# Optimization experiments

Measured on AMD Instinct MI355X. Metric: run time of the kernel, lower is better.

Reference implementation:

```python
import jax, jax.numpy as jnp
import numpy as np

B, H, W = 4, 64, 64
INPLANES, PLANES, G, K = 608, 152, 19, 3
KK = K * K
EPS = 1e-5


def conv2d(x, w, stride=1, padding=0, dilation=1):
    return jax.lax.conv_general_dilated(
        x, w, (stride, stride), [(padding, padding)] * 2,
        rhs_dilation=(dilation, dilation),
        dimension_numbers=("NCHW", "OIHW", "NCHW"))


def bn(x, g, b, m, v):
    # inference-mode batchnorm (affine with running stats)
    inv = g / jnp.sqrt(v + EPS)
    return x * inv[None, :, None, None] + (b - m * inv)[None, :, None, None]


def deform_conv(x, offset, w, pad=1, dil=1):
    # x: [B,C,H,W], offset: [B, 2*G*KK, H, W] ((dy,dx) pairs per group per tap), w: [Cout,C,K,K]
    Bs, C, Hh, Ww = x.shape
    Cg = C // G
    off = offset.reshape(Bs, G, KK, 2, Hh, Ww)
    ky, kx = jnp.meshgrid(jnp.arange(K), jnp.arange(K), indexing="ij")
    base_y = (jnp.arange(Hh) - pad)[None, None, None, :, None] + (dil * ky.reshape(-1))[None, None, :, None, None]
    base_x = (jnp.arange(Ww) - pad)[None, None, None, None, :] + (dil * kx.reshape(-1))[None, None, :, None, None]
    ys = base_y + off[:, :, :, 0]  # [B,G,KK,H,W]
    xs = base_x + off[:, :, :, 1]
    y0 = jnp.floor(ys)
    x0 = jnp.floor(xs)
    wy = ys - y0
    wx = xs - x0
    y0i = y0.astype(jnp.int32)
    x0i = x0.astype(jnp.int32)
    xf = x.reshape(Bs, G, Cg, Hh * Ww)

    def gather(yi, xi, wgt):
        valid = ((yi >= 0) & (yi < Hh) & (xi >= 0) & (xi < Ww)).astype(x.dtype)
        idx = jnp.clip(yi, 0, Hh - 1) * Ww + jnp.clip(xi, 0, Ww - 1)
        idxf = jnp.broadcast_to(idx.reshape(Bs, G, 1, KK * Hh * Ww), (Bs, G, Cg, KK * Hh * Ww))
        g = jnp.take_along_axis(xf, idxf, axis=3).reshape(Bs, G, Cg, KK, Hh, Ww)
        return g * (wgt * valid)[:, :, None]

    samp = (gather(y0i, x0i, (1 - wy) * (1 - wx))
            + gather(y0i, x0i + 1, (1 - wy) * wx)
            + gather(y0i + 1, x0i, wy * (1 - wx))
            + gather(y0i + 1, x0i + 1, wy * wx))  # [B,G,Cg,KK,H,W]
    wr = w.reshape(w.shape[0], G, Cg, KK)
    return jnp.einsum("bgckhw,ogck->bohw", samp, wr)


def setup_inputs() -> dict:
    key = jax.random.key(0)
    ks = jax.random.split(key, 8)
    d = {}
    d["x"] = jax.random.normal(ks[0], (B, INPLANES, H, W), jnp.float32)
    d["conv1_w"] = jax.random.normal(ks[1], (PLANES, INPLANES, 1, 1), jnp.float32) * 0.05
    d["conv2_w"] = jax.random.normal(ks[2], (2 * G * KK, PLANES, 3, 3), jnp.float32) * 0.01
    d["dconv_w"] = jax.random.normal(ks[3], (PLANES, PLANES, 3, 3), jnp.float32) * 0.05
    d["conv3_w"] = jax.random.normal(ks[4], (4 * PLANES, PLANES, 1, 1), jnp.float32) * 0.05
    for i, (name, c) in enumerate([("bn1", PLANES), ("bn2", PLANES), ("bn3", 4 * PLANES)]):
        k1, k2, k3, k4 = jax.random.split(ks[5 + i], 4)
        d[name + "_g"] = jax.random.uniform(k1, (c,), jnp.float32, 0.5, 1.5)
        d[name + "_b"] = jax.random.normal(k2, (c,), jnp.float32) * 0.1
        d[name + "_m"] = jax.random.normal(k3, (c,), jnp.float32) * 0.1
        d[name + "_v"] = jax.random.uniform(k4, (c,), jnp.float32, 0.5, 1.5)
    return d


def reference(x, conv1_w, conv2_w, dconv_w, conv3_w,
              bn1_g, bn1_b, bn1_m, bn1_v,
              bn2_g, bn2_b, bn2_m, bn2_v,
              bn3_g, bn3_b, bn3_m, bn3_v):
    out = jax.nn.relu(conv2d(x, conv1_w))           # conv1 -> relu (order as in source)
    out = bn(out, bn1_g, bn1_b, bn1_m, bn1_v)       # -> bn1
    offset = conv2d(out, conv2_w, padding=1)         # offset-generating 3x3 conv
    out = deform_conv(out, offset, dconv_w)          # deformable 3x3 conv
    out = bn(jax.nn.relu(out), bn2_g, bn2_b, bn2_m, bn2_v)
    out = bn(conv2d(out, conv3_w), bn3_g, bn3_b, bn3_m, bn3_v)
    return jax.nn.relu(out + x)
```

## Files before the change

### kernel.cpp

```cpp
#include <hip/hip_runtime.h>

#define EPSV 1e-5f

typedef __bf16 bf16_t;
typedef __bf16 bf16x8 __attribute__((ext_vector_type(8)));
typedef float f32x4 __attribute__((ext_vector_type(4)));

__device__ inline bf16x8 bzero8() {
  bf16x8 z;
#pragma unroll
  for (int i = 0; i < 8; i++) z[i] = (bf16_t)0.f;
  return z;
}

__device__ inline f32x4 mfma16(bf16x8 a, bf16x8 b, f32x4 c) {
  return __builtin_amdgcn_mfma_f32_16x16x32_bf16(a, b, c, 0, 0, 0);
}

#define W1E (160 * 608)
#define W2E (384 * 1376)
#define WDE (192 * 1376)
#define W3E (640 * 160)

__global__ __launch_bounds__(256) void prep_weights(
    const float* __restrict__ w1, const float* __restrict__ w2,
    const float* __restrict__ wd, const float* __restrict__ w3,
    bf16_t* __restrict__ w1b, bf16_t* __restrict__ w2b,
    bf16_t* __restrict__ wdb, bf16_t* __restrict__ w3b) {
  int i = blockIdx.x * 256 + threadIdx.x;
  float v = 0.f;
  if (i < W1E) {
    int oc = i / 608, ic = i % 608;
    if (oc < 152) v = w1[oc * 608 + ic];
    w1b[i] = (bf16_t)v;
  } else if (i < W1E + W2E) {
    int j = i - W1E;
    int oc = j / 1376, k = j % 1376;
    if (oc < 342 && k < 1368) {
      int t = k / 152, ic = k % 152;
      v = w2[(oc * 152 + ic) * 9 + t];
    }
    w2b[j] = (bf16_t)v;
  } else if (i < W1E + W2E + WDE) {
    int j = i - W1E - W2E;
    int o = j / 1376, k = j % 1376;
    if (o < 152 && k < 1368) {
      int t = k / 152, ic = k % 152;
      v = wd[(o * 152 + ic) * 9 + t];
    }
    wdb[j] = (bf16_t)v;
  } else if (i < W1E + W2E + WDE + W3E) {
    int j = i - W1E - W2E - WDE;
    int oc = j / 160, ic = j % 160;
    if (oc < 608 && ic < 152) v = w3[oc * 152 + ic];
    w3b[j] = (bf16_t)v;
  }
}

__global__ void prep_bn(const float* g1, const float* b1, const float* m1, const float* v1,
                        const float* g2, const float* b2, const float* m2, const float* v2,
                        const float* g3, const float* b3, const float* m3, const float* v3,
                        float* __restrict__ bnc) {
  int i = threadIdx.x;
  if (i < 152) {
    float inv = g1[i] / sqrtf(v1[i] + EPSV);
    bnc[i] = inv;
    bnc[152 + i] = b1[i] - m1[i] * inv;
    float inv2 = g2[i] / sqrtf(v2[i] + EPSV);
    bnc[304 + i] = inv2;
    bnc[456 + i] = b2[i] - m2[i] * inv2;
  }
  if (i < 608) {
    float inv3 = g3[i] / sqrtf(v3[i] + EPSV);
    bnc[608 + i] = inv3;
    bnc[1216 + i] = b3[i] - m3[i] * inv3;
  }
}

__global__ __launch_bounds__(256) void s1_conv1(const float* __restrict__ x,
                                                const bf16_t* __restrict__ w1b,
                                                const float* __restrict__ bnc,
                                                bf16_t* __restrict__ out1) {
  __shared__ bf16_t t1[32 * 616];
  int tid = threadIdx.x;
  int px0 = blockIdx.x * 32;
  int b = px0 >> 12, sp0 = px0 & 4095;
  for (int task = tid; task < 608 * 8; task += 256) {
    int c = task >> 3, i4 = task & 7;
    f32x4 v = *(const f32x4*)(x + (((size_t)(b * 608 + c)) << 12) + sp0 + i4 * 4);
#pragma unroll
    for (int i = 0; i < 4; i++) t1[(i4 * 4 + i) * 616 + c] = (bf16_t)v[i];
  }
  __syncthreads();
  int wid = tid >> 6, lane = tid & 63, q = lane >> 4, lr = lane & 15;
  int mw = wid & 1, nw = wid >> 1;
  f32x4 acc[5];
#pragma unroll
  for (int n = 0; n < 5; n++) acc[n] = (f32x4){0.f, 0.f, 0.f, 0.f};
  for (int kk = 0; kk < 19; kk++) {
    int k0 = kk * 32 + q * 8;
    bf16x8 a = *(const bf16x8*)(t1 + (mw * 16 + lr) * 616 + k0);
#pragma unroll
    for (int n = 0; n < 5; n++) {
      bf16x8 bf = *(const bf16x8*)(w1b + (nw * 80 + n * 16 + lr) * 608 + k0);
      acc[n] = mfma16(a, bf, acc[n]);
    }
  }
#pragma unroll
  for (int n = 0; n < 5; n++) {
    int oc = nw * 80 + n * 16 + lr;
    if (oc < 152) {
      float inv = bnc[oc], beta = bnc[152 + oc];
#pragma unroll
      for (int i = 0; i < 4; i++) {
        int p = px0 + mw * 16 + q * 4 + i;
        float v = fmaxf(acc[n][i], 0.f) * inv + beta;
        out1[(size_t)p * 152 + oc] = (bf16_t)v;
      }
    }
  }
}

__global__ __launch_bounds__(256, 4) void s2_offs(const bf16_t* __restrict__ out1,
                                                  const bf16_t* __restrict__ w2b,
                                                  float* __restrict__ offs) {
  __shared__ bf16_t t2[3 * 34 * 156];
  int tid = threadIdx.x;
  int nh = blockIdx.x & 1;
  int rest = blockIdx.x >> 1;
  int xh = rest & 1, y = (rest >> 1) & 63, b = rest >> 7;
  const bf16_t* ob = out1 + (((size_t)b) << 12) * 152;
  int x0 = xh * 32 - 1;
  for (int task = tid; task < 3 * 34 * 19; task += 256) {
    int j = task / 646, r = task % 646;
    int xi = r / 19, cb = r % 19;
    int yy = y + j - 1, xx = x0 + xi;
    bf16x8 v = bzero8();
    if (yy >= 0 && yy < 64 && xx >= 0 && xx < 64)
      v = *(const bf16x8*)(ob + (size_t)(yy * 64 + xx) * 152 + cb * 8);
    *(bf16x8*)(t2 + (j * 34 + xi) * 156 + cb * 8) = v;
  }
  __syncthreads();
  int wid = tid >> 6, lane = tid & 63, q = lane >> 4, lr = lane & 15;
  int ncol0 = nh * 192 + wid * 48;
  f32x4 acc[2][3];
#pragma unroll
  for (int m = 0; m < 2; m++)
#pragma unroll
    for (int n = 0; n < 3; n++) acc[m][n] = (f32x4){0.f, 0.f, 0.f, 0.f};
  const bf16_t* wb = w2b + (size_t)(ncol0 + lr) * 1376;
#pragma unroll
  for (int kk = 0; kk < 43; kk++) {
    int k0 = kk * 32 + q * 8;
    bf16x8 bfr[3];
#pragma unroll
    for (int n = 0; n < 3; n++)
      bfr[n] = *(const bf16x8*)(wb + (size_t)(n * 16) * 1376 + k0);
    bf16x8 a[2];
    if (k0 < 1368) {
      int t = k0 / 152, c0 = k0 - t * 152;
      int dy = t / 3, dxp1 = t - dy * 3;
#pragma unroll
      for (int m = 0; m < 2; m++)
        a[m] = *(const bf16x8*)(t2 + (dy * 34 + m * 16 + lr + dxp1) * 156 + c0);
    } else {
      a[0] = bzero8();
      a[1] = bzero8();
    }
#pragma unroll
    for (int n = 0; n < 3; n++)
#pragma unroll
      for (int m = 0; m < 2; m++) acc[m][n] = mfma16(a[m], bfr[n], acc[m][n]);
  }
#pragma unroll
  for (int n = 0; n < 3; n++) {
    int col = ncol0 + n * 16 + lr;
    if (col < 342) {
#pragma unroll
      for (int m = 0; m < 2; m++)
#pragma unroll
        for (int i = 0; i < 4; i++) {
          int p = (b << 12) + y * 64 + xh * 32 + m * 16 + q * 4 + i;
          offs[(size_t)p * 344 + col] = acc[m][n][i];
        }
    }
  }
}

__global__ __launch_bounds__(256, 8) void s3a_sample(const bf16_t* __restrict__ out1,
                                                     const float* __restrict__ offs,
                                                     bf16_t* __restrict__ samp,
                                                     int p_base) {
  int task = blockIdx.x * 256 + threadIdx.x;
  int lp = task / 171, s = task - lp * 171;
  int t = s / 19, g = s - t * 19;
  int p = p_base + lp;
  int b = p >> 12, y = (p >> 6) & 63, xc = p & 63;
  int ky = t / 3, kx = t - ky * 3;
  float2 ov = *(const float2*)(offs + (size_t)p * 344 + g * 18 + t * 2);
  float ys = (float)(y - 1 + ky) + ov.x;
  float xs = (float)(xc - 1 + kx) + ov.y;
  float y0f = floorf(ys), x0f = floorf(xs);
  float wy = ys - y0f, wx = xs - x0f;
  int y0 = (int)y0f, x0 = (int)x0f;
  int y1 = y0 + 1, x1 = x0 + 1;
  int y0c = min(max(y0, 0), 63), x0c = min(max(x0, 0), 63);
  int y1c = min(max(y1, 0), 63), x1c = min(max(x1, 0), 63);
  float vy0 = (y0 == y0c) ? 1.f : 0.f;
  float vy1 = (y1 == y1c) ? 1.f : 0.f;
  float vx0 = (x0 == x0c) ? 1.f : 0.f;
  float vx1 = (x1 == x1c) ? 1.f : 0.f;
  float w00 = (1.f - wy) * (1.f - wx) * vy0 * vx0;
  float w01 = (1.f - wy) * wx * vy0 * vx1;
  float w10 = wy * (1.f - wx) * vy1 * vx0;
  float w11 = wy * wx * vy1 * vx1;
  const bf16_t* bg = out1 + (((size_t)b << 12) * 152) + g * 8;
  bf16x8 c00 = *(const bf16x8*)(bg + (size_t)(y0c * 64 + x0c) * 152);
  bf16x8 c01 = *(const bf16x8*)(bg + (size_t)(y0c * 64 + x1c) * 152);
  bf16x8 c10 = *(const bf16x8*)(bg + (size_t)(y1c * 64 + x0c) * 152);
  bf16x8 c11 = *(const bf16x8*)(bg + (size_t)(y1c * 64 + x1c) * 152);
  bf16x8 o;
#pragma unroll
  for (int i = 0; i < 8; i++) {
    float f = w00 * (float)c00[i];
    f = fmaf(w01, (float)c01[i], f);
    f = fmaf(w10, (float)c10[i], f);
    f = fmaf(w11, (float)c11[i], f);
    o[i] = (bf16_t)f;
  }
  *(bf16x8*)(samp + (size_t)lp * 1376 + t * 152 + g * 8) = o;
  if (s == 170) *(bf16x8*)(samp + (size_t)lp * 1376 + 1368) = bzero8();
}

__global__ __launch_bounds__(512, 4) void s3b_gemm(const bf16_t* __restrict__ samp,
                                                   const bf16_t* __restrict__ wdb,
                                                   const float* __restrict__ bnc,
                                                   bf16_t* __restrict__ a2,
                                                   int p_base) {
  int tid = threadIdx.x;
  int wid = tid >> 6, lane = tid & 63, q = lane >> 4, lr = lane & 15;
  int mw = wid & 1, nw = wid >> 1;
  int lrow = blockIdx.x * 32 + mw * 16;
  const bf16_t* arow = samp + (size_t)(lrow + lr) * 1376;
  const bf16_t* wb = wdb + (size_t)(nw * 48 + lr) * 1376;
  f32x4 acc[3];
#pragma unroll
  for (int n = 0; n < 3; n++) acc[n] = (f32x4){0.f, 0.f, 0.f, 0.f};
#pragma unroll
  for (int kk = 0; kk < 43; kk++) {
    int k0 = kk * 32 + q * 8;
    bf16x8 a = *(const bf16x8*)(arow + k0);
#pragma unroll
    for (int n = 0; n < 3; n++) {
      bf16x8 bf = *(const bf16x8*)(wb + (size_t)(n * 16) * 1376 + k0);
      acc[n] = mfma16(a, bf, acc[n]);
    }
  }
#pragma unroll
  for (int n = 0; n < 3; n++) {
    int oc = nw * 48 + n * 16 + lr;
    if (oc < 152) {
      float inv = bnc[304 + oc], beta = bnc[456 + oc];
#pragma unroll
      for (int i = 0; i < 4; i++) {
        int p = p_base + lrow + q * 4 + i;
        float v = fmaxf(acc[n][i], 0.f) * inv + beta;
        a2[(size_t)p * 152 + oc] = (bf16_t)v;
      }
    }
  }
}

__global__ __launch_bounds__(256) void s4_conv3(const bf16_t* __restrict__ a2,
                                                const bf16_t* __restrict__ w3b,
                                                const float* __restrict__ bnc,
                                                const float* __restrict__ x,
                                                float* __restrict__ out) {
  int tid = threadIdx.x;
  int wid = tid >> 6, lane = tid & 63, q = lane >> 4, lr = lane & 15;
  int p0 = blockIdx.x * 16;
  int b = p0 >> 12, sp0 = p0 & 4095;
  f32x4 acc[10];
#pragma unroll
  for (int n = 0; n < 10; n++) acc[n] = (f32x4){0.f, 0.f, 0.f, 0.f};
  for (int kk = 0; kk < 5; kk++) {
    int k0 = kk * 32 + q * 8;
    bf16x8 a = (k0 < 152) ? *(const bf16x8*)(a2 + (size_t)(p0 + lr) * 152 + k0) : bzero8();
#pragma unroll
    for (int n = 0; n < 10; n++) {
      bf16x8 bf = *(const bf16x8*)(w3b + (size_t)(wid * 160 + n * 16 + lr) * 160 + k0);
      acc[n] = mfma16(a, bf, acc[n]);
    }
  }
#pragma unroll
  for (int n = 0; n < 10; n++) {
    int oc = wid * 160 + n * 16 + lr;
    if (oc < 608) {
      float inv = bnc[608 + oc], beta = bnc[1216 + oc];
      size_t gi = (((size_t)(b * 608 + oc)) << 12) + sp0 + q * 4;
      f32x4 xr = *(const f32x4*)(x + gi);
      f32x4 o;
#pragma unroll
      for (int i = 0; i < 4; i++) o[i] = fmaxf(acc[n][i] * inv + beta + xr[i], 0.f);
      *(f32x4*)(out + gi) = o;
    }
  }
}

extern "C" void kernel_launch(void* const* d_in, const int* in_sizes, int n_in,
                              void* d_out, int out_size, void* d_ws, size_t ws_size,
                              hipStream_t stream) {
  const float* x = (const float*)d_in[0];
  const float* w1 = (const float*)d_in[1];
  const float* w2 = (const float*)d_in[2];
  const float* wd = (const float*)d_in[3];
  const float* w3 = (const float*)d_in[4];
  const float* g1 = (const float*)d_in[5];
  const float* b1 = (const float*)d_in[6];
  const float* m1 = (const float*)d_in[7];
  const float* v1 = (const float*)d_in[8];
  const float* g2 = (const float*)d_in[9];
  const float* b2 = (const float*)d_in[10];
  const float* m2 = (const float*)d_in[11];
  const float* v2 = (const float*)d_in[12];
  const float* g3 = (const float*)d_in[13];
  const float* b3 = (const float*)d_in[14];
  const float* m3 = (const float*)d_in[15];
  const float* v3 = (const float*)d_in[16];

  char* ws = (char*)d_ws;
  bf16_t* w1b = (bf16_t*)(ws + 0);
  bf16_t* w2b = (bf16_t*)(ws + 194560);
  bf16_t* wdb = (bf16_t*)(ws + 1251328);
  bf16_t* w3b = (bf16_t*)(ws + 1779712);
  float* bnc = (float*)(ws + 1984512);
  bf16_t* out1 = (bf16_t*)(ws + 1991808);
  float* offs = (float*)(ws + 6972544);
  bf16_t* a2 = (bf16_t*)(ws + 29516928);
  bf16_t* samp = (bf16_t*)(ws + 34497664);
  float* out = (float*)d_out;

  prep_weights<<<3876, 256, 0, stream>>>(w1, w2, wd, w3, w1b, w2b, wdb, w3b);
  prep_bn<<<1, 640, 0, stream>>>(g1, b1, m1, v1, g2, b2, m2, v2, g3, b3, m3, v3, bnc);
  s1_conv1<<<512, 256, 0, stream>>>(x, w1b, bnc, out1);
  s2_offs<<<1024, 256, 0, stream>>>(out1, w2b, offs);

  size_t base = 34497664;
  int nchunk = 1;
  if (ws_size < base + (size_t)16384 * 1376 * 2) nchunk = 4;
  if (nchunk == 4 && ws_size < base + (size_t)4096 * 1376 * 2) nchunk = 16;
  int npix = 16384 / nchunk;
  for (int c = 0; c < nchunk; c++) {
    s3a_sample<<<npix * 171 / 256, 256, 0, stream>>>(out1, offs, samp, c * npix);
    s3b_gemm<<<npix / 32, 512, 0, stream>>>(samp, wdb, bnc, a2, c * npix);
  }

  s4_conv3<<<1024, 256, 0, stream>>>(a2, w3b, bnc, x, out);
}
```

Measured before the change: 182.4 us.

## Fuse deformable sampling with GEMM via LDS and split-K partials reduced in conv3

Bilinear sampling and the deformable-conv GEMM now run in one kernel. Each block samples 16 pixels times 3 taps into shared memory and runs the MFMA on them, so the large bf16 sample buffer is never written to or read back from global memory. The K dimension is split three ways across blocks, which writes fp32 partial sums. conv3 then sums the partials and applies relu and bn2 on the fly. In exchange it adds fp32 partial traffic (3x16384x192 floats), a per-element bn lookup in conv3, and weight re-reads from global memory per small tile.

```diff
diff --git a/kernel.cpp b/kernel.cpp
--- a/kernel.cpp
+++ b/kernel.cpp
@@ -5,6 +5,7 @@
 typedef __bf16 bf16_t;
 typedef __bf16 bf16x8 __attribute__((ext_vector_type(8)));
 typedef float f32x4 __attribute__((ext_vector_type(4)));
+typedef float f32x8 __attribute__((ext_vector_type(8)));
 
 __device__ inline bf16x8 bzero8() {
   bf16x8 z;
@@ -19,7 +20,7 @@
 
 #define W1E (160 * 608)
 #define W2E (384 * 1376)
-#define WDE (192 * 1376)
+#define WDE (192 * 1440)
 #define W3E (640 * 160)
 
 __global__ __launch_bounds__(256) void prep_weights(
@@ -43,11 +44,9 @@
     w2b[j] = (bf16_t)v;
   } else if (i < W1E + W2E + WDE) {
     int j = i - W1E - W2E;
-    int o = j / 1376, k = j % 1376;
-    if (o < 152 && k < 1368) {
-      int t = k / 152, ic = k % 152;
-      v = wd[(o * 152 + ic) * 9 + t];
-    }
+    int o = j / 1440, k = j % 1440;
+    int t = k / 160, ic = k % 160;
+    if (o < 152 && ic < 152) v = wd[(o * 152 + ic) * 9 + t];
     wdb[j] = (bf16_t)v;
   } else if (i < W1E + W2E + WDE + W3E) {
     int j = i - W1E - W2E - WDE;
@@ -187,105 +186,123 @@
   }
 }
 
-__global__ __launch_bounds__(256, 8) void s3a_sample(const bf16_t* __restrict__ out1,
-                                                     const float* __restrict__ offs,
-                                                     bf16_t* __restrict__ samp,
-                                                     int p_base) {
-  int task = blockIdx.x * 256 + threadIdx.x;
-  int lp = task / 171, s = task - lp * 171;
-  int t = s / 19, g = s - t * 19;
-  int p = p_base + lp;
-  int b = p >> 12, y = (p >> 6) & 63, xc = p & 63;
-  int ky = t / 3, kx = t - ky * 3;
-  float2 ov = *(const float2*)(offs + (size_t)p * 344 + g * 18 + t * 2);
-  float ys = (float)(y - 1 + ky) + ov.x;
-  float xs = (float)(xc - 1 + kx) + ov.y;
-  float y0f = floorf(ys), x0f = floorf(xs);
-  float wy = ys - y0f, wx = xs - x0f;
-  int y0 = (int)y0f, x0 = (int)x0f;
-  int y1 = y0 + 1, x1 = x0 + 1;
-  int y0c = min(max(y0, 0), 63), x0c = min(max(x0, 0), 63);
-  int y1c = min(max(y1, 0), 63), x1c = min(max(x1, 0), 63);
-  float vy0 = (y0 == y0c) ? 1.f : 0.f;
-  float vy1 = (y1 == y1c) ? 1.f : 0.f;
-  float vx0 = (x0 == x0c) ? 1.f : 0.f;
-  float vx1 = (x1 == x1c) ? 1.f : 0.f;
-  float w00 = (1.f - wy) * (1.f - wx) * vy0 * vx0;
-  float w01 = (1.f - wy) * wx * vy0 * vx1;
-  float w10 = wy * (1.f - wx) * vy1 * vx0;
-  float w11 = wy * wx * vy1 * vx1;
-  const bf16_t* bg = out1 + (((size_t)b << 12) * 152) + g * 8;
-  bf16x8 c00 = *(const bf16x8*)(bg + (size_t)(y0c * 64 + x0c) * 152);
-  bf16x8 c01 = *(const bf16x8*)(bg + (size_t)(y0c * 64 + x1c) * 152);
-  bf16x8 c10 = *(const bf16x8*)(bg + (size_t)(y1c * 64 + x0c) * 152);
-  bf16x8 c11 = *(const bf16x8*)(bg + (size_t)(y1c * 64 + x1c) * 152);
-  bf16x8 o;
-#pragma unroll
-  for (int i = 0; i < 8; i++) {
-    float f = w00 * (float)c00[i];
-    f = fmaf(w01, (float)c01[i], f);
-    f = fmaf(w10, (float)c10[i], f);
-    f = fmaf(w11, (float)c11[i], f);
-    o[i] = (bf16_t)f;
-  }
-  *(bf16x8*)(samp + (size_t)lp * 1376 + t * 152 + g * 8) = o;
-  if (s == 170) *(bf16x8*)(samp + (size_t)lp * 1376 + 1368) = bzero8();
-}
-
-__global__ __launch_bounds__(512, 4) void s3b_gemm(const bf16_t* __restrict__ samp,
+__global__ __launch_bounds__(256, 8) void s3_dconv(const bf16_t* __restrict__ out1,
+                                                   const float* __restrict__ offs,
                                                    const bf16_t* __restrict__ wdb,
-                                                   const float* __restrict__ bnc,
-                                                   bf16_t* __restrict__ a2,
-                                                   int p_base) {
+                                                   float* __restrict__ p3) {
+  __shared__ bf16_t abuf[16 * 488];
   int tid = threadIdx.x;
+  int bi = blockIdx.x;
+  int kc = bi % 3, pt = bi / 3;
+  int row0 = pt * 16;
+  int bb = row0 >> 12;
+  const bf16_t* obase = out1 + (((size_t)bb << 12) * 152);
+  if (tid < 64) {
+    int t = tid >> 4, r = tid & 15;
+    int off = (t < 3) ? t * 160 + 152 : 480;
+    *(bf16x8*)(abuf + r * 488 + off) = bzero8();
+  }
+  int t0 = kc * 3;
+  for (int task = tid; task < 912; task += 256) {
+    int tl = task / 304;
+    int rem = task - tl * 304;
+    int r = rem / 19, g = rem - r * 19;
+    int t = t0 + tl;
+    int ky = t / 3, kx = t - ky * 3;
+    int p = row0 + r;
+    int y = (p >> 6) & 63, xc = p & 63;
+    float2 ov = *(const float2*)(offs + (size_t)p * 344 + g * 18 + t * 2);
+    float ys = (float)(y - 1 + ky) + ov.x;
+    float xs = (float)(xc - 1 + kx) + ov.y;
+    float y0f = floorf(ys), x0f = floorf(xs);
+    float wy = ys - y0f, wx = xs - x0f;
+    int y0 = (int)y0f, x0 = (int)x0f;
+    int y1 = y0 + 1, x1 = x0 + 1;
+    int y0c = min(max(y0, 0), 63), x0c = min(max(x0, 0), 63);
+    int y1c = min(max(y1, 0), 63), x1c = min(max(x1, 0), 63);
+    float vy0 = (y0 == y0c) ? 1.f : 0.f;
+    float vy1 = (y1 == y1c) ? 1.f : 0.f;
+    float vx0 = (x0 == x0c) ? 1.f : 0.f;
+    float vx1 = (x1 == x1c) ? 1.f : 0.f;
+    float w00 = (1.f - wy) * (1.f - wx) * vy0 * vx0;
+    float w01 = (1.f - wy) * wx * vy0 * vx1;
+    float w10 = wy * (1.f - wx) * vy1 * vx0;
+    float w11 = wy * wx * vy1 * vx1;
+    const bf16_t* bg = obase + g * 8;
+    bf16x8 c00 = *(const bf16x8*)(bg + (size_t)(y0c * 64 + x0c) * 152);
+    bf16x8 c01 = *(const bf16x8*)(bg + (size_t)(y0c * 64 + x1c) * 152);
+    bf16x8 c10 = *(const bf16x8*)(bg + (size_t)(y1c * 64 + x0c) * 152);
+    bf16x8 c11 = *(const bf16x8*)(bg + (size_t)(y1c * 64 + x1c) * 152);
+    bf16x8 o;
+#pragma unroll
+    for (int i = 0; i < 8; i++) {
+      float f = w00 * (float)c00[i];
+      f = fmaf(w01, (float)c01[i], f);
+      f = fmaf(w10, (float)c10[i], f);
+      f = fmaf(w11, (float)c11[i], f);
+      o[i] = (bf16_t)f;
+    }
+    *(bf16x8*)(abuf + r * 488 + tl * 160 + g * 8) = o;
+  }
+  __syncthreads();
   int wid = tid >> 6, lane = tid & 63, q = lane >> 4, lr = lane & 15;
-  int mw = wid & 1, nw = wid >> 1;
-  int lrow = blockIdx.x * 32 + mw * 16;
-  const bf16_t* arow = samp + (size_t)(lrow + lr) * 1376;
-  const bf16_t* wb = wdb + (size_t)(nw * 48 + lr) * 1376;
   f32x4 acc[3];
 #pragma unroll
   for (int n = 0; n < 3; n++) acc[n] = (f32x4){0.f, 0.f, 0.f, 0.f};
-#pragma unroll
-  for (int kk = 0; kk < 43; kk++) {
+  const bf16_t* wb = wdb + (size_t)(wid * 48 + lr) * 1440 + kc * 480;
+#pragma unroll
+  for (int kk = 0; kk < 15; kk++) {
     int k0 = kk * 32 + q * 8;
-    bf16x8 a = *(const bf16x8*)(arow + k0);
+    bf16x8 a = *(const bf16x8*)(abuf + lr * 488 + k0);
 #pragma unroll
     for (int n = 0; n < 3; n++) {
-      bf16x8 bf = *(const bf16x8*)(wb + (size_t)(n * 16) * 1376 + k0);
+      bf16x8 bf = *(const bf16x8*)(wb + (size_t)(n * 16) * 1440 + k0);
       acc[n] = mfma16(a, bf, acc[n]);
     }
   }
+  float* pp = p3 + ((size_t)kc * 16384 + row0) * 192;
 #pragma unroll
   for (int n = 0; n < 3; n++) {
-    int oc = nw * 48 + n * 16 + lr;
-    if (oc < 152) {
-      float inv = bnc[304 + oc], beta = bnc[456 + oc];
-#pragma unroll
-      for (int i = 0; i < 4; i++) {
-        int p = p_base + lrow + q * 4 + i;
-        float v = fmaxf(acc[n][i], 0.f) * inv + beta;
-        a2[(size_t)p * 152 + oc] = (bf16_t)v;
-      }
-    }
-  }
-}
-
-__global__ __launch_bounds__(256) void s4_conv3(const bf16_t* __restrict__ a2,
+    int col = wid * 48 + n * 16 + lr;
+#pragma unroll
+    for (int i = 0; i < 4; i++) {
+      int rr = q * 4 + i;
+      pp[(size_t)rr * 192 + col] = acc[n][i];
+    }
+  }
+}
+
+__global__ __launch_bounds__(256) void s4_conv3(const float* __restrict__ p3,
                                                 const bf16_t* __restrict__ w3b,
                                                 const float* __restrict__ bnc,
                                                 const float* __restrict__ x,
                                                 float* __restrict__ out) {
+  const size_t PSZ = (size_t)16384 * 192;
   int tid = threadIdx.x;
   int wid = tid >> 6, lane = tid & 63, q = lane >> 4, lr = lane & 15;
   int p0 = blockIdx.x * 16;
   int b = p0 >> 12, sp0 = p0 & 4095;
+  const float* pbase = p3 + (size_t)(p0 + lr) * 192;
   f32x4 acc[10];
 #pragma unroll
   for (int n = 0; n < 10; n++) acc[n] = (f32x4){0.f, 0.f, 0.f, 0.f};
+#pragma unroll
   for (int kk = 0; kk < 5; kk++) {
     int k0 = kk * 32 + q * 8;
-    bf16x8 a = (k0 < 152) ? *(const bf16x8*)(a2 + (size_t)(p0 + lr) * 152 + k0) : bzero8();
+    bf16x8 a;
+    if (k0 < 152) {
+      f32x8 s0 = *(const f32x8*)(pbase + k0);
+      f32x8 s1 = *(const f32x8*)(pbase + PSZ + k0);
+      f32x8 s2 = *(const f32x8*)(pbase + 2 * PSZ + k0);
+#pragma unroll
+      for (int i = 0; i < 8; i++) {
+        float s = s0[i] + s1[i] + s2[i];
+        float v = fmaxf(s, 0.f) * bnc[304 + k0 + i] + bnc[456 + k0 + i];
+        a[i] = (bf16_t)v;
+      }
+    } else {
+      a = bzero8();
+    }
 #pragma unroll
     for (int n = 0; n < 10; n++) {
       bf16x8 bf = *(const bf16x8*)(w3b + (size_t)(wid * 160 + n * 16 + lr) * 160 + k0);
@@ -332,28 +349,17 @@
   bf16_t* w1b = (bf16_t*)(ws + 0);
   bf16_t* w2b = (bf16_t*)(ws + 194560);
   bf16_t* wdb = (bf16_t*)(ws + 1251328);
-  bf16_t* w3b = (bf16_t*)(ws + 1779712);
-  float* bnc = (float*)(ws + 1984512);
-  bf16_t* out1 = (bf16_t*)(ws + 1991808);
-  float* offs = (float*)(ws + 6972544);
-  bf16_t* a2 = (bf16_t*)(ws + 29516928);
-  bf16_t* samp = (bf16_t*)(ws + 34497664);
+  bf16_t* w3b = (bf16_t*)(ws + 1804288);
+  float* bnc = (float*)(ws + 2009088);
+  bf16_t* out1 = (bf16_t*)(ws + 2016384);
+  float* offs = (float*)(ws + 6997120);
+  float* p3 = (float*)(ws + 29541504);
   float* out = (float*)d_out;
 
-  prep_weights<<<3876, 256, 0, stream>>>(w1, w2, wd, w3, w1b, w2b, wdb, w3b);
+  prep_weights<<<3924, 256, 0, stream>>>(w1, w2, wd, w3, w1b, w2b, wdb, w3b);
   prep_bn<<<1, 640, 0, stream>>>(g1, b1, m1, v1, g2, b2, m2, v2, g3, b3, m3, v3, bnc);
   s1_conv1<<<512, 256, 0, stream>>>(x, w1b, bnc, out1);
   s2_offs<<<1024, 256, 0, stream>>>(out1, w2b, offs);
-
-  size_t base = 34497664;
-  int nchunk = 1;
-  if (ws_size < base + (size_t)16384 * 1376 * 2) nchunk = 4;
-  if (nchunk == 4 && ws_size < base + (size_t)4096 * 1376 * 2) nchunk = 16;
-  int npix = 16384 / nchunk;
-  for (int c = 0; c < nchunk; c++) {
-    s3a_sample<<<npix * 171 / 256, 256, 0, stream>>>(out1, offs, samp, c * npix);
-    s3b_gemm<<<npix / 32, 512, 0, stream>>>(samp, wdb, bnc, a2, c * npix);
-  }
-
-  s4_conv3<<<1024, 256, 0, stream>>>(a2, w3b, bnc, x, out);
-}
+  s3_dconv<<<3072, 256, 0, stream>>>(out1, offs, wdb, p3);
+  s4_conv3<<<1024, 256, 0, stream>>>(p3, w3b, bnc, x, out);
+}
```

Result: slower. 194.7 us (+6.8%).

## Stage deform-conv GEMM A tiles in LDS with double buffering per tap

Applied to the files above, without the earlier changes.

The sampled-activation matrix is re-laid out so each of the 9 taps has its own 160-wide padded segment. The deformable-conv GEMM now stages each tap's 32-row A tile into double-buffered shared memory, so one block of 4 waves shares it. Each wave computes 32 rows by 48 columns, which doubles reuse of the weight fragments it loads from global memory. The chunked sample/GEMM loop and its workspace-size check are gone: the code now assumes the workspace can hold the full 16384x1440 buffer, and a2 reuses the out1 region. The trade-off is fewer waves per block, extra barriers, and a larger buffer written and read.

```diff
diff --git a/kernel.cpp b/kernel.cpp
--- a/kernel.cpp
+++ b/kernel.cpp
@@ -19,7 +19,7 @@
 
 #define W1E (160 * 608)
 #define W2E (384 * 1376)
-#define WDE (192 * 1376)
+#define WDE (192 * 1440)
 #define W3E (640 * 160)
 
 __global__ __launch_bounds__(256) void prep_weights(
@@ -43,11 +43,9 @@
     w2b[j] = (bf16_t)v;
   } else if (i < W1E + W2E + WDE) {
     int j = i - W1E - W2E;
-    int o = j / 1376, k = j % 1376;
-    if (o < 152 && k < 1368) {
-      int t = k / 152, ic = k % 152;
-      v = wd[(o * 152 + ic) * 9 + t];
-    }
+    int o = j / 1440, k = j % 1440;
+    int t = k / 160, ic = k % 160;
+    if (o < 152 && ic < 152) v = wd[(o * 152 + ic) * 9 + t];
     wdb[j] = (bf16_t)v;
   } else if (i < W1E + W2E + WDE + W3E) {
     int j = i - W1E - W2E - WDE;
@@ -189,15 +187,13 @@
 
 __global__ __launch_bounds__(256, 8) void s3a_sample(const bf16_t* __restrict__ out1,
                                                      const float* __restrict__ offs,
-                                                     bf16_t* __restrict__ samp,
-                                                     int p_base) {
+                                                     bf16_t* __restrict__ samp) {
   int task = blockIdx.x * 256 + threadIdx.x;
   int lp = task / 171, s = task - lp * 171;
   int t = s / 19, g = s - t * 19;
-  int p = p_base + lp;
-  int b = p >> 12, y = (p >> 6) & 63, xc = p & 63;
+  int b = lp >> 12, y = (lp >> 6) & 63, xc = lp & 63;
   int ky = t / 3, kx = t - ky * 3;
-  float2 ov = *(const float2*)(offs + (size_t)p * 344 + g * 18 + t * 2);
+  float2 ov = *(const float2*)(offs + (size_t)lp * 344 + g * 18 + t * 2);
   float ys = (float)(y - 1 + ky) + ov.x;
   float xs = (float)(xc - 1 + kx) + ov.y;
   float y0f = floorf(ys), x0f = floorf(xs);
@@ -228,45 +224,77 @@
     f = fmaf(w11, (float)c11[i], f);
     o[i] = (bf16_t)f;
   }
-  *(bf16x8*)(samp + (size_t)lp * 1376 + t * 152 + g * 8) = o;
-  if (s == 170) *(bf16x8*)(samp + (size_t)lp * 1376 + 1368) = bzero8();
-}
-
-__global__ __launch_bounds__(512, 4) void s3b_gemm(const bf16_t* __restrict__ samp,
+  *(bf16x8*)(samp + (size_t)lp * 1440 + t * 160 + g * 8) = o;
+  if (g == 18) *(bf16x8*)(samp + (size_t)lp * 1440 + t * 160 + 152) = bzero8();
+}
+
+__global__ __launch_bounds__(256, 4) void s3b_gemm(const bf16_t* __restrict__ samp,
                                                    const bf16_t* __restrict__ wdb,
                                                    const float* __restrict__ bnc,
-                                                   bf16_t* __restrict__ a2,
-                                                   int p_base) {
+                                                   bf16_t* __restrict__ a2) {
+  __shared__ bf16_t at[2][32 * 168];
   int tid = threadIdx.x;
+  int row0 = blockIdx.x * 32;
   int wid = tid >> 6, lane = tid & 63, q = lane >> 4, lr = lane & 15;
-  int mw = wid & 1, nw = wid >> 1;
-  int lrow = blockIdx.x * 32 + mw * 16;
-  const bf16_t* arow = samp + (size_t)(lrow + lr) * 1376;
-  const bf16_t* wb = wdb + (size_t)(nw * 48 + lr) * 1376;
-  f32x4 acc[3];
-#pragma unroll
-  for (int n = 0; n < 3; n++) acc[n] = (f32x4){0.f, 0.f, 0.f, 0.f};
-#pragma unroll
-  for (int kk = 0; kk < 43; kk++) {
-    int k0 = kk * 32 + q * 8;
-    bf16x8 a = *(const bf16x8*)(arow + k0);
-#pragma unroll
-    for (int n = 0; n < 3; n++) {
-      bf16x8 bf = *(const bf16x8*)(wb + (size_t)(n * 16) * 1376 + k0);
-      acc[n] = mfma16(a, bf, acc[n]);
-    }
-  }
+  f32x4 acc[2][3];
+#pragma unroll
+  for (int m = 0; m < 2; m++)
+#pragma unroll
+    for (int n = 0; n < 3; n++) acc[m][n] = (f32x4){0.f, 0.f, 0.f, 0.f};
+  const bf16_t* wb = wdb + (size_t)(wid * 48 + lr) * 1440;
+  const bf16_t* arow = samp + (size_t)row0 * 1440;
+
+#define STAGE(T, BUF)                                                        \
+  for (int task = tid; task < 640; task += 256) {                            \
+    int r = task / 20, c8 = task - r * 20;                                   \
+    *(bf16x8*)(at[BUF] + r * 168 + c8 * 8) =                                 \
+        *(const bf16x8*)(arow + (size_t)r * 1440 + (T)*160 + c8 * 8);        \
+  }
+
+#define TAP(T, BUF)                                                          \
+  {                                                                          \
+    if ((T) < 8) STAGE((T) + 1, (BUF) ^ 1)                                   \
+    _Pragma("unroll") for (int kk = 0; kk < 5; kk++) {                       \
+      int k0 = kk * 32 + q * 8;                                              \
+      bf16x8 a0 = *(const bf16x8*)(at[BUF] + lr * 168 + k0);                 \
+      bf16x8 a1 = *(const bf16x8*)(at[BUF] + (16 + lr) * 168 + k0);          \
+      _Pragma("unroll") for (int n = 0; n < 3; n++) {                        \
+        bf16x8 bf =                                                          \
+            *(const bf16x8*)(wb + (size_t)(n * 16) * 1440 + (T)*160 + k0);   \
+        acc[0][n] = mfma16(a0, bf, acc[0][n]);                               \
+        acc[1][n] = mfma16(a1, bf, acc[1][n]);                               \
+      }                                                                      \
+    }                                                                        \
+    __syncthreads();                                                         \
+  }
+
+  STAGE(0, 0)
+  __syncthreads();
+  TAP(0, 0)
+  TAP(1, 1)
+  TAP(2, 0)
+  TAP(3, 1)
+  TAP(4, 0)
+  TAP(5, 1)
+  TAP(6, 0)
+  TAP(7, 1)
+  TAP(8, 0)
+#undef TAP
+#undef STAGE
+
 #pragma unroll
   for (int n = 0; n < 3; n++) {
-    int oc = nw * 48 + n * 16 + lr;
+    int oc = wid * 48 + n * 16 + lr;
     if (oc < 152) {
       float inv = bnc[304 + oc], beta = bnc[456 + oc];
 #pragma unroll
-      for (int i = 0; i < 4; i++) {
-        int p = p_base + lrow + q * 4 + i;
-        float v = fmaxf(acc[n][i], 0.f) * inv + beta;
-        a2[(size_t)p * 152 + oc] = (bf16_t)v;
-      }
+      for (int m = 0; m < 2; m++)
+#pragma unroll
+        for (int i = 0; i < 4; i++) {
+          int p = row0 + m * 16 + q * 4 + i;
+          float v = fmaxf(acc[m][n][i], 0.f) * inv + beta;
+          a2[(size_t)p * 152 + oc] = (bf16_t)v;
+        }
     }
   }
 }
@@ -332,28 +360,19 @@
   bf16_t* w1b = (bf16_t*)(ws + 0);
   bf16_t* w2b = (bf16_t*)(ws + 194560);
   bf16_t* wdb = (bf16_t*)(ws + 1251328);
-  bf16_t* w3b = (bf16_t*)(ws + 1779712);
-  float* bnc = (float*)(ws + 1984512);
-  bf16_t* out1 = (bf16_t*)(ws + 1991808);
-  float* offs = (float*)(ws + 6972544);
-  bf16_t* a2 = (bf16_t*)(ws + 29516928);
-  bf16_t* samp = (bf16_t*)(ws + 34497664);
+  bf16_t* w3b = (bf16_t*)(ws + 1804288);
+  float* bnc = (float*)(ws + 2009088);
+  bf16_t* out1 = (bf16_t*)(ws + 2016384);
+  float* offs = (float*)(ws + 6997120);
+  bf16_t* samp = (bf16_t*)(ws + 29541504);
+  bf16_t* a2 = (bf16_t*)(ws + 2016384);
   float* out = (float*)d_out;
 
-  prep_weights<<<3876, 256, 0, stream>>>(w1, w2, wd, w3, w1b, w2b, wdb, w3b);
+  prep_weights<<<3924, 256, 0, stream>>>(w1, w2, wd, w3, w1b, w2b, wdb, w3b);
   prep_bn<<<1, 640, 0, stream>>>(g1, b1, m1, v1, g2, b2, m2, v2, g3, b3, m3, v3, bnc);
   s1_conv1<<<512, 256, 0, stream>>>(x, w1b, bnc, out1);
   s2_offs<<<1024, 256, 0, stream>>>(out1, w2b, offs);
-
-  size_t base = 34497664;
-  int nchunk = 1;
-  if (ws_size < base + (size_t)16384 * 1376 * 2) nchunk = 4;
-  if (nchunk == 4 && ws_size < base + (size_t)4096 * 1376 * 2) nchunk = 16;
-  int npix = 16384 / nchunk;
-  for (int c = 0; c < nchunk; c++) {
-    s3a_sample<<<npix * 171 / 256, 256, 0, stream>>>(out1, offs, samp, c * npix);
-    s3b_gemm<<<npix / 32, 512, 0, stream>>>(samp, wdb, bnc, a2, c * npix);
-  }
-
+  s3a_sample<<<10944, 256, 0, stream>>>(out1, offs, samp);
+  s3b_gemm<<<512, 256, 0, stream>>>(samp, wdb, bnc, a2);
   s4_conv3<<<1024, 256, 0, stream>>>(a2, w3b, bnc, x, out);
 }
```

Measured after the change: 180.1 us. Within noise of the previous version (-1.2%).
